# Kernel tuning notes

Measured on AMD Instinct MI355X. Metric: run time of the kernel, lower is better.

The kernel has to match this reference:

```python
import jax, jax.numpy as jnp
import numpy as np

K = 32
D = 256


def setup_inputs() -> dict:
    key = jax.random.key(0)
    k1, k2, kW, kV, kb = jax.random.split(key, 5)
    B, L1, L2 = 16, 256, 256
    x1 = jax.random.normal(k1, (B, L1, D), dtype=jnp.float32)
    x2 = jax.random.normal(k2, (B, L2, D), dtype=jnp.float32)
    # kaiming_uniform-style init bounds
    bound_W = np.sqrt(6.0 / ((1 + 5) * D))  # fan_in = d, a=sqrt(5)
    W = jax.random.uniform(kW, (K, D, D), minval=-bound_W, maxval=bound_W, dtype=jnp.float32)
    bound_V = np.sqrt(6.0 / ((1 + 5) * 2 * D))
    V = jax.random.uniform(kV, (K, 2 * D), minval=-bound_V, maxval=bound_V, dtype=jnp.float32)
    bound_b = 1.0 / np.sqrt(2 * D)
    b = jax.random.uniform(kb, (K,), minval=-bound_b, maxval=bound_b, dtype=jnp.float32)
    return {"x1": x1, "x2": x2, "W": W, "V": V, "b": b}


def reference(x1, x2, W, V, b):
    # x1: [B,L1,d], x2: [B,L2,d], W: [k,d,d], V: [k,2d], b: [k]
    d = x1.shape[-1]
    # bilinear term: (x1 W) x2^T per output channel k -> [B,k,L1,L2]
    temp = jnp.einsum('bld,kde->bkle', x1, W)            # [B,k,L1,d]
    bilinear_out = jnp.einsum('bkle,bme->bklm', temp, x2)  # [B,k,L1,L2]
    # linear term: V @ concat(x1,x2) = V1 x1 + V2 x2, broadcast-summed
    V1, V2 = V[:, :d], V[:, d:]
    lin1 = jnp.einsum('bld,kd->bkl', x1, V1)             # [B,k,L1]
    lin2 = jnp.einsum('bmd,kd->bkm', x2, V2)             # [B,k,L2]
    linear_out = lin1[:, :, :, None] + lin2[:, :, None, :] + b[None, :, None, None]
    return jax.nn.relu(bilinear_out + linear_out)
```

## Files before the change

### kernel.cpp

```cpp
#include <hip/hip_runtime.h>
#include <hip/hip_bf16.h>

typedef unsigned short u16;
typedef unsigned short ushort8v __attribute__((ext_vector_type(8)));
typedef __bf16 bf16x8 __attribute__((ext_vector_type(8)));
typedef float f32x4 __attribute__((ext_vector_type(4)));

#define NB 16
#define NK 32
#define ND 256
#define NL 256

__device__ __forceinline__ u16 f2bf(float f) {
    __hip_bfloat16 h = __float2bfloat16(f);
    return __builtin_bit_cast(u16, h);
}

__device__ __forceinline__ bf16x8 pack8(float4 a, float4 b) {
    ushort8v u;
    u[0] = f2bf(a.x); u[1] = f2bf(a.y); u[2] = f2bf(a.z); u[3] = f2bf(a.w);
    u[4] = f2bf(b.x); u[5] = f2bf(b.y); u[6] = f2bf(b.z); u[7] = f2bf(b.w);
    return __builtin_bit_cast(bf16x8, u);
}

__device__ __forceinline__ void gload_lds16(const void* g, void* l) {
    __builtin_amdgcn_global_load_lds(
        (const __attribute__((address_space(1))) unsigned int*)g,
        (__attribute__((address_space(3))) unsigned int*)l, 16, 0, 0);
}


__global__ void prep_kernel(const float* __restrict__ x1, const float* __restrict__ x2,
                            const float* __restrict__ W, const float* __restrict__ V,
                            const float* __restrict__ bb,
                            u16* __restrict__ x1f, u16* __restrict__ x2f, u16* __restrict__ Wf,
                            float* __restrict__ lin1, float* __restrict__ lin2) {
    int bid = blockIdx.x;
    int tid = threadIdx.x;
    if (bid < 4096) {
        const float* src; u16* dst; long f4;
        if (bid < 1024)      { src = x1; dst = x1f; f4 = (long)bid * 256 + tid; }
        else if (bid < 2048) { src = x2; dst = x2f; f4 = (long)(bid - 1024) * 256 + tid; }
        else                 { src = W;  dst = Wf;  f4 = (long)(bid - 2048) * 256 + tid; }
        long idx = f4 << 2;
        int mat = (int)(idx >> 16);
        int r = (int)((idx >> 8) & 255);
        int c = (int)(idx & 255);
        float4 v = ((const float4*)src)[f4];
        ushort4 o;
        o.x = f2bf(v.x); o.y = f2bf(v.y); o.z = f2bf(v.z); o.w = f2bf(v.w);
        int rt = r >> 4, ct = c >> 5;
        int lane = (r & 15) | (((c >> 3) & 3) << 4);
        long off = ((long)mat << 16) + (((rt << 3) + ct) << 9) + (lane << 3) + (c & 7);
        *(ushort4*)(dst + off) = o;
        return;
    }
    int bid2 = bid - 4096;
    int b = bid2 >> 1, pass = bid2 & 1;
    int lane = tid & 63;
    int wv   = tid >> 6;
    int lrow = lane & 15;
    int lk8  = (lane >> 4) << 3;
    int j4   = (lane >> 4) << 2;
    int lbase = wv << 6;

    const f32x4 fz = {0.f, 0.f, 0.f, 0.f};
    const float* xp = (pass ? x2 : x1) + ((long)b << 16);
    const float* vp = V + (pass ? ND : 0);
    f32x4 acc[4][2];
#pragma unroll
    for (int i = 0; i < 4; ++i) { acc[i][0] = fz; acc[i][1] = fz; }
#pragma unroll
    for (int dt = 0; dt < 8; ++dt) {
        int d = (dt << 5) + lk8;
        bf16x8 af[4], bf[2];
#pragma unroll
        for (int lt = 0; lt < 4; ++lt) {
            const float4* s = (const float4*)(xp + ((long)((lbase + (lt << 4) + lrow)) << 8) + d);
            af[lt] = pack8(s[0], s[1]);
        }
#pragma unroll
        for (int nt = 0; nt < 2; ++nt) {
            const float4* s = (const float4*)(vp + (long)((nt << 4) + lrow) * (2 * ND) + d);
            bf[nt] = pack8(s[0], s[1]);
        }
#pragma unroll
        for (int nt = 0; nt < 2; ++nt)
#pragma unroll
            for (int lt = 0; lt < 4; ++lt)
                acc[lt][nt] = __builtin_amdgcn_mfma_f32_16x16x32_bf16(af[lt], bf[nt], acc[lt][nt], 0, 0, 0);
    }
    float* dst = (pass ? lin2 : lin1) + ((long)b << 13);
#pragma unroll
    for (int nt = 0; nt < 2; ++nt) {
        int kk = (nt << 4) + lrow;
        float add = pass ? 0.f : bb[kk];
#pragma unroll
        for (int lt = 0; lt < 4; ++lt) {
            float4 v;
            v.x = acc[lt][nt][0] + add; v.y = acc[lt][nt][1] + add;
            v.z = acc[lt][nt][2] + add; v.w = acc[lt][nt][3] + add;
            *(float4*)(dst + ((long)kk << 8) + lbase + (lt << 4) + j4) = v;
        }
    }
}

__launch_bounds__(512, 6)
__global__ void ntn_main(const u16* __restrict__ x1f, const u16* __restrict__ x2f,
                         const u16* __restrict__ Wf,
                         const float* __restrict__ lin1, const float* __restrict__ lin2,
                         float* __restrict__ out) {
    __shared__ __align__(16) char ldsRaw[32768];

    int bid = blockIdx.x;
    int xcd   = bid & 7;
    int j     = bid >> 3;
    int slot  = j >> 7;
    int inner = j & 127;
    int st    = (slot << 3) | xcd;
    int kg = st >> 2, bg = st & 3;
    int k  = (kg << 3) | (inner >> 4);
    int b  = (bg << 2) | ((inner >> 2) & 3);
    int mq = inner & 3;

    int tid  = threadIdx.x;
    int lane = tid & 63;
    int wid  = tid >> 6;
    int lrow = lane & 15;
    int j4   = (lane >> 4) << 2;

    {
        const char* src = (const char*)(x2f + ((long)b << 16) + ((long)mq << 14));
#pragma unroll
        for (int it = 0; it < 4; ++it) {
            int chunk = (it << 3) + wid;
            gload_lds16(src + (chunk << 10) + (lane << 4), ldsRaw + (chunk << 10));
        }
    }

    f32x4 acc[4][2];
    const f32x4 fz = {0.f, 0.f, 0.f, 0.f};
#pragma unroll
    for (int i = 0; i < 4; ++i) { acc[i][0] = fz; acc[i][1] = fz; }

    __syncthreads();

    {
        int wrA = wid >> 1;
        int wcA = wid & 1;
        const u16* wp = Wf + ((long)k << 16);
#pragma unroll
        for (int et = 0; et < 8; ++et) {
            bf16x8 af[4], bfr[2];
#pragma unroll
            for (int lt = 0; lt < 4; ++lt)
                af[lt] = *(const bf16x8*)(wp + (((((wrA << 2) + lt) << 3) + et) << 9) + (lane << 3));
#pragma unroll
            for (int nt = 0; nt < 2; ++nt)
                bfr[nt] = *(const bf16x8*)(ldsRaw + ((((((wcA << 1) + nt) << 3) + et) << 10) + (lane << 4)));
#pragma unroll
            for (int nt = 0; nt < 2; ++nt)
#pragma unroll
                for (int lt = 0; lt < 4; ++lt)
                    acc[lt][nt] = __builtin_amdgcn_mfma_f32_16x16x32_bf16(af[lt], bfr[nt], acc[lt][nt], 0, 0, 0);
        }
    }
    __syncthreads();

    {
        int wrA = wid >> 1;
        int wcA = wid & 1;
#pragma unroll
        for (int lt = 0; lt < 4; ++lt) {
            int d0 = (wrA << 6) + (lt << 4) + j4;
#pragma unroll
            for (int nt = 0; nt < 2; ++nt) {
                int m = (wcA << 5) + (nt << 4) + lrow;
                ushort4 pk;
                pk.x = f2bf(acc[lt][nt][0]);
                pk.y = f2bf(acc[lt][nt][1]);
                pk.z = f2bf(acc[lt][nt][2]);
                pk.w = f2bf(acc[lt][nt][3]);
                *(ushort4*)(ldsRaw + (m << 9) + ((d0 << 1) ^ ((m & 7) << 4))) = pk;
            }
        }
    }
    __syncthreads();

#pragma unroll
    for (int i = 0; i < 4; ++i) { acc[i][0] = fz; acc[i][1] = fz; }

    {
        const u16* x1p = x1f + ((long)b << 16);
        int lk8 = (lane >> 4) << 3;
#pragma unroll
        for (int dt = 0; dt < 8; ++dt) {
            int d = (dt << 5) + lk8;
            bf16x8 am[4], xl[2];
#pragma unroll
            for (int mt = 0; mt < 4; ++mt) {
                int m = (mt << 4) + lrow;
                am[mt] = *(const bf16x8*)(ldsRaw + (m << 9) + ((d << 1) ^ ((m & 7) << 4)));
            }
#pragma unroll
            for (int lt = 0; lt < 2; ++lt)
                xl[lt] = *(const bf16x8*)(x1p + (((((wid << 1) + lt) << 3) + dt) << 9) + (lane << 3));
#pragma unroll
            for (int lt = 0; lt < 2; ++lt)
#pragma unroll
                for (int mt = 0; mt < 4; ++mt)
                    acc[mt][lt] = __builtin_amdgcn_mfma_f32_16x16x32_bf16(am[mt], xl[lt], acc[mt][lt], 0, 0, 0);
        }
    }
    __syncthreads();

    {
        const float* l1p = lin1 + (((long)(b * NK + k)) << 8);
        const float* l2p = lin2 + (((long)(b * NK + k)) << 8) + (mq << 6);
        float* outp = out + (((long)(b * NK + k)) << 16) + (mq << 6);

#pragma unroll
        for (int c = 0; c < 2; ++c) {
            if ((wid >> 2) == c) {
                float rb[2];
#pragma unroll
                for (int lt = 0; lt < 2; ++lt)
                    rb[lt] = l1p[(wid << 5) + (lt << 4) + lrow];
#pragma unroll
                for (int mt = 0; mt < 4; ++mt) {
                    int mcol = (mt << 4) + j4;
                    float4 l2v = *(const float4*)(l2p + mcol);
#pragma unroll
                    for (int lt = 0; lt < 2; ++lt) {
                        int row = ((wid & 3) << 5) + (lt << 4) + lrow;
                        f32x4 v;
                        v[0] = acc[mt][lt][0] + rb[lt] + l2v.x;
                        v[1] = acc[mt][lt][1] + rb[lt] + l2v.y;
                        v[2] = acc[mt][lt][2] + rb[lt] + l2v.z;
                        v[3] = acc[mt][lt][3] + rb[lt] + l2v.w;
                        v[0] = v[0] > 0.f ? v[0] : 0.f;
                        v[1] = v[1] > 0.f ? v[1] : 0.f;
                        v[2] = v[2] > 0.f ? v[2] : 0.f;
                        v[3] = v[3] > 0.f ? v[3] : 0.f;
                        *(f32x4*)(ldsRaw + (row << 8) + ((mcol << 2) ^ ((row & 7) << 4))) = v;
                    }
                }
            }
            __syncthreads();
#pragma unroll
            for (int it = 0; it < 4; ++it) {
                int g = (it << 9) + tid;
                int row = g >> 4;
                int c4  = g & 15;
                f32x4 v = *(const f32x4*)(ldsRaw + (row << 8) + ((c4 << 4) ^ ((row & 7) << 4)));
                __builtin_nontemporal_store(v, (f32x4*)(outp + ((long)((c << 7) + row) << 8) + (c4 << 2)));
            }
            if (c == 0) __syncthreads();
        }
    }
}

extern "C" void kernel_launch(void* const* d_in, const int* in_sizes, int n_in,
                              void* d_out, int out_size, void* d_ws, size_t ws_size,
                              hipStream_t stream) {
    const float* x1 = (const float*)d_in[0];
    const float* x2 = (const float*)d_in[1];
    const float* W  = (const float*)d_in[2];
    const float* V  = (const float*)d_in[3];
    const float* bb = (const float*)d_in[4];
    float* out = (float*)d_out;

    char* ws = (char*)d_ws;
    u16*   x1f  = (u16*)(ws);
    u16*   x2f  = (u16*)(ws + (2l << 20));
    u16*   Wf   = (u16*)(ws + (4l << 20));
    float* lin1 = (float*)(ws + (8l << 20));
    float* lin2 = (float*)(ws + (8l << 20) + (512l << 10));

    hipLaunchKernelGGL(prep_kernel, dim3(4128), dim3(256), 0, stream,
                       x1, x2, W, V, bb, x1f, x2f, Wf, lin1, lin2);
    hipLaunchKernelGGL(ntn_main, dim3(2048), dim3(512), 0, stream,
                       x1f, x2f, Wf, lin1, lin2, out);
}
```

Before: 72.96 us.

## Pipeline second GEMM in row chunks overlapping output stores with compute

Splits the second GEMM (U·x1ᵀ) into four 64-row chunks. Each chunk's epilogue goes into a separate 16KB LDS staging buffer, and its global stores are issued while the next chunk's MFMAs run. The x1 fragments for a chunk are loaded into registers up front, and the full-block syncthreads are replaced by lgkmcnt-only barriers. This aims to overlap the output write traffic with compute and shrink accumulator register use, at the cost of 16KB more LDS per block, which may lower occupancy, plus more barriers.

```diff
diff --git a/kernel.cpp b/kernel.cpp
--- a/kernel.cpp
+++ b/kernel.cpp
@@ -27,6 +27,12 @@
     __builtin_amdgcn_global_load_lds(
         (const __attribute__((address_space(1))) unsigned int*)g,
         (__attribute__((address_space(3))) unsigned int*)l, 16, 0, 0);
+}
+
+__device__ __forceinline__ void barrier_lgkm() {
+    asm volatile("s_waitcnt lgkmcnt(0)" ::: "memory");
+    __builtin_amdgcn_s_barrier();
+    asm volatile("" ::: "memory");
 }
 
 
@@ -110,7 +116,8 @@
                          const u16* __restrict__ Wf,
                          const float* __restrict__ lin1, const float* __restrict__ lin2,
                          float* __restrict__ out) {
-    __shared__ __align__(16) char ldsRaw[32768];
+    __shared__ __align__(16) char ldsU[32768];
+    __shared__ __align__(16) char ldsE[16384];
 
     int bid = blockIdx.x;
     int xcd   = bid & 7;
@@ -127,6 +134,7 @@
     int lane = tid & 63;
     int wid  = tid >> 6;
     int lrow = lane & 15;
+    int lk8  = (lane >> 4) << 3;
     int j4   = (lane >> 4) << 2;
 
     {
@@ -134,14 +142,14 @@
 #pragma unroll
         for (int it = 0; it < 4; ++it) {
             int chunk = (it << 3) + wid;
-            gload_lds16(src + (chunk << 10) + (lane << 4), ldsRaw + (chunk << 10));
-        }
-    }
-
-    f32x4 acc[4][2];
+            gload_lds16(src + (chunk << 10) + (lane << 4), ldsU + (chunk << 10));
+        }
+    }
+
     const f32x4 fz = {0.f, 0.f, 0.f, 0.f};
-#pragma unroll
-    for (int i = 0; i < 4; ++i) { acc[i][0] = fz; acc[i][1] = fz; }
+    f32x4 accA[4][2];
+#pragma unroll
+    for (int i = 0; i < 4; ++i) { accA[i][0] = fz; accA[i][1] = fz; }
 
     __syncthreads();
 
@@ -157,12 +165,12 @@
                 af[lt] = *(const bf16x8*)(wp + (((((wrA << 2) + lt) << 3) + et) << 9) + (lane << 3));
 #pragma unroll
             for (int nt = 0; nt < 2; ++nt)
-                bfr[nt] = *(const bf16x8*)(ldsRaw + ((((((wcA << 1) + nt) << 3) + et) << 10) + (lane << 4)));
+                bfr[nt] = *(const bf16x8*)(ldsU + ((((((wcA << 1) + nt) << 3) + et) << 10) + (lane << 4)));
 #pragma unroll
             for (int nt = 0; nt < 2; ++nt)
 #pragma unroll
                 for (int lt = 0; lt < 4; ++lt)
-                    acc[lt][nt] = __builtin_amdgcn_mfma_f32_16x16x32_bf16(af[lt], bfr[nt], acc[lt][nt], 0, 0, 0);
+                    accA[lt][nt] = __builtin_amdgcn_mfma_f32_16x16x32_bf16(af[lt], bfr[nt], accA[lt][nt], 0, 0, 0);
         }
     }
     __syncthreads();
@@ -177,85 +185,92 @@
             for (int nt = 0; nt < 2; ++nt) {
                 int m = (wcA << 5) + (nt << 4) + lrow;
                 ushort4 pk;
-                pk.x = f2bf(acc[lt][nt][0]);
-                pk.y = f2bf(acc[lt][nt][1]);
-                pk.z = f2bf(acc[lt][nt][2]);
-                pk.w = f2bf(acc[lt][nt][3]);
-                *(ushort4*)(ldsRaw + (m << 9) + ((d0 << 1) ^ ((m & 7) << 4))) = pk;
+                pk.x = f2bf(accA[lt][nt][0]);
+                pk.y = f2bf(accA[lt][nt][1]);
+                pk.z = f2bf(accA[lt][nt][2]);
+                pk.w = f2bf(accA[lt][nt][3]);
+                *(ushort4*)(ldsU + (m << 9) + ((d0 << 1) ^ ((m & 7) << 4))) = pk;
             }
         }
     }
     __syncthreads();
 
-#pragma unroll
-    for (int i = 0; i < 4; ++i) { acc[i][0] = fz; acc[i][1] = fz; }
-
     {
         const u16* x1p = x1f + ((long)b << 16);
-        int lk8 = (lane >> 4) << 3;
-#pragma unroll
-        for (int dt = 0; dt < 8; ++dt) {
-            int d = (dt << 5) + lk8;
-            bf16x8 am[4], xl[2];
-#pragma unroll
-            for (int mt = 0; mt < 4; ++mt) {
-                int m = (mt << 4) + lrow;
-                am[mt] = *(const bf16x8*)(ldsRaw + (m << 9) + ((d << 1) ^ ((m & 7) << 4)));
-            }
-#pragma unroll
-            for (int lt = 0; lt < 2; ++lt)
-                xl[lt] = *(const bf16x8*)(x1p + (((((wid << 1) + lt) << 3) + dt) << 9) + (lane << 3));
-#pragma unroll
-            for (int lt = 0; lt < 2; ++lt)
-#pragma unroll
-                for (int mt = 0; mt < 4; ++mt)
-                    acc[mt][lt] = __builtin_amdgcn_mfma_f32_16x16x32_bf16(am[mt], xl[lt], acc[mt][lt], 0, 0, 0);
-        }
-    }
-    __syncthreads();
-
-    {
+        int ltq = wid & 3;
+        int mp  = wid >> 2;
         const float* l1p = lin1 + (((long)(b * NK + k)) << 8);
         const float* l2p = lin2 + (((long)(b * NK + k)) << 8) + (mq << 6);
         float* outp = out + (((long)(b * NK + k)) << 16) + (mq << 6);
 
-#pragma unroll
-        for (int c = 0; c < 2; ++c) {
-            if ((wid >> 2) == c) {
-                float rb[2];
-#pragma unroll
-                for (int lt = 0; lt < 2; ++lt)
-                    rb[lt] = l1p[(wid << 5) + (lt << 4) + lrow];
-#pragma unroll
-                for (int mt = 0; mt < 4; ++mt) {
-                    int mcol = (mt << 4) + j4;
-                    float4 l2v = *(const float4*)(l2p + mcol);
-#pragma unroll
-                    for (int lt = 0; lt < 2; ++lt) {
-                        int row = ((wid & 3) << 5) + (lt << 4) + lrow;
-                        f32x4 v;
-                        v[0] = acc[mt][lt][0] + rb[lt] + l2v.x;
-                        v[1] = acc[mt][lt][1] + rb[lt] + l2v.y;
-                        v[2] = acc[mt][lt][2] + rb[lt] + l2v.z;
-                        v[3] = acc[mt][lt][3] + rb[lt] + l2v.w;
-                        v[0] = v[0] > 0.f ? v[0] : 0.f;
-                        v[1] = v[1] > 0.f ? v[1] : 0.f;
-                        v[2] = v[2] > 0.f ? v[2] : 0.f;
-                        v[3] = v[3] > 0.f ? v[3] : 0.f;
-                        *(f32x4*)(ldsRaw + (row << 8) + ((mcol << 2) ^ ((row & 7) << 4))) = v;
-                    }
+        float4 l2v[2];
+        l2v[0] = *(const float4*)(l2p + (mp << 5) + j4);
+        l2v[1] = *(const float4*)(l2p + (mp << 5) + 16 + j4);
+
+#pragma unroll
+        for (int q = 0; q < 4; ++q) {
+            bf16x8 xl[8];
+#pragma unroll
+            for (int dt = 0; dt < 8; ++dt)
+                xl[dt] = *(const bf16x8*)(x1p + ((((((q << 2) + ltq) << 3) + dt) << 9)) + (lane << 3));
+            __builtin_amdgcn_sched_barrier(0);
+
+            if (q > 0) {
+#pragma unroll
+                for (int it = 0; it < 2; ++it) {
+                    int g = (it << 9) + tid;
+                    int row = g >> 4;
+                    int c4  = g & 15;
+                    f32x4 v = *(const f32x4*)(ldsE + (row << 8) + ((c4 << 4) ^ ((row & 7) << 4)));
+                    __builtin_nontemporal_store(v,
+                        (f32x4*)(outp + ((long)(((q - 1) << 6) + row) << 8) + (c4 << 2)));
                 }
             }
-            __syncthreads();
-#pragma unroll
-            for (int it = 0; it < 4; ++it) {
-                int g = (it << 9) + tid;
-                int row = g >> 4;
-                int c4  = g & 15;
-                f32x4 v = *(const f32x4*)(ldsRaw + (row << 8) + ((c4 << 4) ^ ((row & 7) << 4)));
-                __builtin_nontemporal_store(v, (f32x4*)(outp + ((long)((c << 7) + row) << 8) + (c4 << 2)));
-            }
-            if (c == 0) __syncthreads();
+
+            f32x4 acc[2] = {fz, fz};
+#pragma unroll
+            for (int dt = 0; dt < 8; ++dt) {
+                int d = (dt << 5) + lk8;
+#pragma unroll
+                for (int mt = 0; mt < 2; ++mt) {
+                    int m = (mp << 5) + (mt << 4) + lrow;
+                    bf16x8 am = *(const bf16x8*)(ldsU + (m << 9) + ((d << 1) ^ ((m & 7) << 4)));
+                    acc[mt] = __builtin_amdgcn_mfma_f32_16x16x32_bf16(am, xl[dt], acc[mt], 0, 0, 0);
+                }
+            }
+
+            barrier_lgkm();
+
+            {
+                float rb = l1p[(q << 6) + (ltq << 4) + lrow];
+                int row = (ltq << 4) + lrow;
+#pragma unroll
+                for (int mt = 0; mt < 2; ++mt) {
+                    int mloc = (mp << 5) + (mt << 4) + j4;
+                    f32x4 v;
+                    v[0] = acc[mt][0] + rb + l2v[mt].x;
+                    v[1] = acc[mt][1] + rb + l2v[mt].y;
+                    v[2] = acc[mt][2] + rb + l2v[mt].z;
+                    v[3] = acc[mt][3] + rb + l2v[mt].w;
+                    v[0] = v[0] > 0.f ? v[0] : 0.f;
+                    v[1] = v[1] > 0.f ? v[1] : 0.f;
+                    v[2] = v[2] > 0.f ? v[2] : 0.f;
+                    v[3] = v[3] > 0.f ? v[3] : 0.f;
+                    *(f32x4*)(ldsE + (row << 8) + ((mloc << 2) ^ ((row & 7) << 4))) = v;
+                }
+            }
+
+            barrier_lgkm();
+        }
+
+#pragma unroll
+        for (int it = 0; it < 2; ++it) {
+            int g = (it << 9) + tid;
+            int row = g >> 4;
+            int c4  = g & 15;
+            f32x4 v = *(const f32x4*)(ldsE + (row << 8) + ((c4 << 4) ^ ((row & 7) << 4)));
+            __builtin_nontemporal_store(v,
+                (f32x4*)(outp + ((long)((3 << 6) + row) << 8) + (c4 << 2)));
         }
     }
 }
```

After: 76.25 us. 4.5% more time.
